# Kernel tuning notes

Hardware: AMD Instinct MI355X
Metric: run time of the kernel (lower is better)

The kernel has to match this reference:

```python
import jax, jax.numpy as jnp
import numpy as np

# irreps multiplicities
MUL0_N, MUL1_N = 64, 32   # node:   64x0e + 32x1o  -> dim 160
MUL0_E, MUL1_E = 8, 8     # edge:    8x0e +  8x1o  -> dim 32
MUL0_H, MUL1_H = 64, 32   # hidden: 64x0e + 32x1o  -> dim 160
N_NODES, N_EDGES = 50000, 800000
D_NODE = MUL0_N + 3 * MUL1_N
D_EDGE = MUL0_E + 3 * MUL1_E
D_HID = MUL0_H + 3 * MUL1_H


def _split(x, mul0, mul1):
    # split flat irreps feature into scalars [.., mul0] and vectors [.., mul1, 3]
    s = x[..., :mul0]
    v = x[..., mul0:].reshape(x.shape[0], mul1, 3)
    return s, v


def fctp_messages(x, e, W1, W2, W3, W4):
    """FullyConnectedTensorProduct(node_irreps, edge_irreps -> hidden_irreps), l<=1.
    Paths: (0e,0e->0e), (1o,1o->0e: delta/sqrt3), (0e,1o->1o), (1o,0e->1o)."""
    xs, xv = _split(x, MUL0_N, MUL1_N)   # [E,64], [E,32,3]
    es, ev = _split(e, MUL0_E, MUL1_E)   # [E,8],  [E,8,3]
    inv_sqrt2 = 1.0 / np.sqrt(2.0)       # 2 paths per output irrep
    s1 = jnp.einsum('ea,eb,abc->ec', xs, es, W1) * (1.0 / np.sqrt(MUL0_N * MUL0_E))
    s2 = jnp.einsum('eai,ebi,abc->ec', xv, ev, W2) * (1.0 / (np.sqrt(3.0) * np.sqrt(MUL1_N * MUL1_E)))
    out_s = (s1 + s2) * inv_sqrt2                         # [E,64]
    v1 = jnp.einsum('ea,ebi,abc->eci', xs, ev, W3) * (1.0 / np.sqrt(MUL0_N * MUL1_E))
    v2 = jnp.einsum('eai,eb,abc->eci', xv, es, W4) * (1.0 / np.sqrt(MUL1_N * MUL0_E))
    out_v = (v1 + v2) * inv_sqrt2                         # [E,32,3]
    return jnp.concatenate([out_s, out_v.reshape(out_v.shape[0], -1)], axis=-1)  # [E,160]


def setup_inputs() -> dict:
    key = jax.random.key(0)
    ks = jax.random.split(key, 12)
    node_features = jax.random.normal(ks[0], (N_NODES, D_NODE), dtype=jnp.float32)
    edge_index = jax.random.randint(ks[1], (2, N_EDGES), 0, N_NODES, dtype=jnp.int64)
    edge_attr_tensor = jax.random.normal(ks[2], (N_EDGES, D_EDGE), dtype=jnp.float32)
    node_attr_scalar_raw = jax.random.normal(ks[3], (N_NODES, 1), dtype=jnp.float32)
    # FCTP path weights (mul_in1, mul_in2, mul_out)
    W1 = jax.random.normal(ks[4], (MUL0_N, MUL0_E, MUL0_H), dtype=jnp.float32)
    W2 = jax.random.normal(ks[5], (MUL1_N, MUL1_E, MUL0_H), dtype=jnp.float32)
    W3 = jax.random.normal(ks[6], (MUL0_N, MUL1_E, MUL1_H), dtype=jnp.float32)
    W4 = jax.random.normal(ks[7], (MUL1_N, MUL0_E, MUL1_H), dtype=jnp.float32)
    # runtime-fallback dense layers (Gate raises at runtime in the original)
    Wm = jax.random.normal(ks[8], (D_HID, D_HID), dtype=jnp.float32) / np.sqrt(D_HID)
    bm = jnp.zeros((D_HID,), dtype=jnp.float32)
    Wu = jax.random.normal(ks[9], (D_NODE + D_HID, D_NODE), dtype=jnp.float32) / np.sqrt(D_NODE + D_HID)
    bu = jnp.zeros((D_NODE,), dtype=jnp.float32)
    return {"node_features": node_features, "edge_index": edge_index,
            "edge_attr_tensor": edge_attr_tensor, "node_attr_scalar_raw": node_attr_scalar_raw,
            "W1": W1, "W2": W2, "W3": W3, "W4": W4,
            "Wm": Wm, "bm": bm, "Wu": Wu, "bu": bu}


def reference(node_features, edge_index, edge_attr_tensor, node_attr_scalar_raw,
              W1, W2, W3, W4, Wm, bm, Wu, bu):
    row, col = edge_index[0], edge_index[1]
    # gather source nodes + equivariant tensor-product message
    tp = fctp_messages(node_features[col], edge_attr_tensor, W1, W2, W3, W4)  # [E,160]
    messages = tp @ Wm + bm                                                   # [E,160]
    # scatter-sum aggregation to destination nodes
    agg = jax.ops.segment_sum(messages, row, num_segments=N_NODES)            # [N,160]
    # update (runtime fallback: linear on concat) + residual
    upd = jnp.concatenate([node_features, agg], axis=-1) @ Wu + bu            # [N,160]
    return node_features + upd
```

## Files before the change

kernel.cpp:

```cpp
#include <hip/hip_runtime.h>
#include <hip/hip_bf16.h>

#define NN 50000
#define NE 800000
#define DN 160
#define DE 32
#define NP 50176

typedef __attribute__((ext_vector_type(2))) _Float16 f16x2;
typedef __attribute__((ext_vector_type(8))) _Float16 f16x8;
typedef __attribute__((ext_vector_type(4))) float f32x4;
typedef __attribute__((ext_vector_type(4))) unsigned short u16x4;

#define R2 0.81649658092772603f
#define R4 1.41421356237309515f
#define SC (1.0f/32.0f)

#define XST 172
#define EST 38

union AF { f16x2 p[4]; f16x8 v; };

__device__ __forceinline__ unsigned short f16bits(float f) {
    union { _Float16 h; unsigned short s; } u;
    u.h = (_Float16)f;
    return u.s;
}

__global__ __launch_bounds__(256) void xprep_kernel(const float* __restrict__ x,
                                                    unsigned short* __restrict__ xb) {
    int i = blockIdx.x * 256 + threadIdx.x;
    if (i < NN * DN / 4) {
        const float4 v = reinterpret_cast<const float4*>(x)[i];
        u16x4 p; p[0] = f16bits(v.x); p[1] = f16bits(v.y); p[2] = f16bits(v.z); p[3] = f16bits(v.w);
        reinterpret_cast<u16x4*>(xb)[i] = p;
    }
}

__global__ __launch_bounds__(256) void zero_kernel(float* __restrict__ T,
                                                   int* __restrict__ cnt) {
    int i = blockIdx.x * 256 + threadIdx.x;
    if (i < NN * DN) T[i] = 0.0f;
    if (i < NP) cnt[i] = 0;
}

__global__ __launch_bounds__(256) void hist_kernel(const int* __restrict__ eidx,
                                                   int* __restrict__ cnt) {
    int e = blockIdx.x * 256 + threadIdx.x;
    if (e < NE) atomicAdd(&cnt[eidx[e]], 1);
}

__global__ __launch_bounds__(256) void scan1_kernel(const int* __restrict__ cnt,
                                                    int* __restrict__ cursor,
                                                    int* __restrict__ bsum) {
    __shared__ int s[256];
    const int t = threadIdx.x;
    const int i = blockIdx.x * 256 + t;
    const int v = cnt[i];
    s[t] = v; __syncthreads();
    for (int off = 1; off < 256; off <<= 1) {
        int u = (t >= off) ? s[t - off] : 0;
        __syncthreads(); s[t] += u; __syncthreads();
    }
    cursor[i] = s[t] - v;
    if (t == 255) bsum[blockIdx.x] = s[255];
}

__global__ __launch_bounds__(256) void scan2_kernel(int* __restrict__ bsum) {
    __shared__ int s[256];
    const int t = threadIdx.x;
    const int v = (t < 196) ? bsum[t] : 0;
    s[t] = v; __syncthreads();
    for (int off = 1; off < 256; off <<= 1) {
        int u = (t >= off) ? s[t - off] : 0;
        __syncthreads(); s[t] += u; __syncthreads();
    }
    if (t < 196) bsum[t] = s[t] - v;
}

__global__ __launch_bounds__(256) void scan3_kernel(int* __restrict__ cursor,
                                                    const int* __restrict__ bsum) {
    int i = blockIdx.x * 256 + threadIdx.x;
    cursor[i] += bsum[blockIdx.x];
}

__global__ __launch_bounds__(256) void scatter_kernel(const int* __restrict__ eidx,
                                                      int* __restrict__ cursor,
                                                      int* __restrict__ sorted) {
    int e = blockIdx.x * 256 + threadIdx.x;
    if (e < NE) {
        int pos = atomicAdd(&cursor[eidx[e]], 1);
        sorted[pos] = e;
    }
}

__global__ __launch_bounds__(256) void wprep_edge_kernel(
    const float* __restrict__ W1, const float* __restrict__ W2,
    const float* __restrict__ W3, const float* __restrict__ W4,
    unsigned short* __restrict__ Wh)
{
    int id = blockIdx.x * 256 + threadIdx.x;
    if (id >= 73728) return;
    int j = id & 7, l = (id >> 3) & 63, st = id >> 9;
    int tt = st / 6, s = st % 6;
    int k = 32 * tt + 8 * (l >> 4) + j;
    float w;
    if (s < 4) {
        int c = s * 16 + (l & 15);
        if (k < 512) { int a = k >> 3, b = k & 7; w = W1[(a*8+b)*64 + c] * SC; }
        else { int k2 = k - 512; int a = k2 >> 3, b = k2 & 7; w = W2[(a*8+b)*64 + c] * (R2*SC); }
    } else {
        int c = (s - 4) * 16 + (l & 15);
        if (k < 512) { int a = k >> 3, b = k & 7; w = W3[(a*8+b)*32 + c] * SC; }
        else { int k2 = k - 512; int a = k2 >> 3, b = k2 & 7; w = W4[(a*8+b)*32 + c] * (R4*SC); }
    }
    Wh[id] = f16bits(w);
}

__global__ __launch_bounds__(256) void wcomp_kernel(
    const float* __restrict__ Wm, const float* __restrict__ bm,
    const float* __restrict__ Wu, float* __restrict__ Wc, float* __restrict__ bc)
{
    int id = blockIdx.x * 256 + threadIdx.x;
    if (id < 160 * 160) {
        int k = id / 160, c = id % 160;
        float s = 0.0f;
        for (int h = 0; h < 160; ++h) s = fmaf(Wm[k*160 + h], Wu[(160 + h)*160 + c], s);
        Wc[id] = s;
    }
    if (id < 160) {
        float s = 0.0f;
        for (int h = 0; h < 160; ++h) s = fmaf(bm[h], Wu[(160 + h)*160 + id], s);
        bc[id] = s;
    }
}

__global__ __launch_bounds__(256) void wprep_node_kernel(
    const float* __restrict__ Wu, const float* __restrict__ Wc,
    unsigned short* __restrict__ Wn)
{
    int id = blockIdx.x * 256 + threadIdx.x;
    if (id >= 51200) return;
    int j = id & 7, l = (id >> 3) & 63, tn = id >> 9;
    int tk = tn % 10, n16 = tn / 10;
    int c = n16 * 16 + (l & 15);
    int k = 32 * tk + 8 * (l >> 4) + j;
    float w;
    if (k < 160) {
        w = Wu[k * 160 + c];
    } else {
        int tcol = k - 160;
        int orig = (tcol < 64) ? tcol : 64 + ((tcol - 64) & 31) * 3 + ((tcol - 64) >> 5);
        w = Wc[orig * 160 + c];
    }
    Wn[id] = f16bits(w);
}

template<int UXB>
__global__ __launch_bounds__(256, 3) void edge_kernel(
    const float* __restrict__ x, const unsigned short* __restrict__ xb,
    const int* __restrict__ eidx, const float* __restrict__ ea,
    const unsigned short* __restrict__ Wh,
    const int* __restrict__ sorted, float* __restrict__ T)
{
    __shared__ __align__(16) char smem[64*XST*2 + 64*EST*2];
    __shared__ int rowls[64];
    __shared__ int colls[64];
    __shared__ int sels[64];

    unsigned short* xls = (unsigned short*)smem;
    unsigned short* els = (unsigned short*)(smem + 64*XST*2);

    const int t = threadIdx.x;
    const int base = blockIdx.x * 64;

    if (t < 64) {
        const int se = sorted[base + t];
        sels[t] = se;
        rowls[t] = eidx[se];
        colls[t] = eidx[NE + se];
    }
    __syncthreads();

    if (UXB) {
        for (int j = t; j < 64 * 40; j += 256) {
            int m = j / 40, q = j - m * 40;
            const u16x4 v = *reinterpret_cast<const u16x4*>(xb + (size_t)colls[m] * DN + q * 4);
            *reinterpret_cast<u16x4*>(&xls[m*XST + q*4]) = v;
        }
    } else {
        for (int j = t; j < 64 * 40; j += 256) {
            int m = j / 40, q = j - m * 40;
            const float4 v = *reinterpret_cast<const float4*>(x + (size_t)colls[m] * DN + q * 4);
            u16x4 p; p[0] = f16bits(v.x); p[1] = f16bits(v.y); p[2] = f16bits(v.z); p[3] = f16bits(v.w);
            *reinterpret_cast<u16x4*>(&xls[m*XST + q*4]) = p;
        }
    }
    for (int j = t; j < 64 * 8; j += 256) {
        int m = j >> 3, q = j & 7;
        const float4 v = *reinterpret_cast<const float4*>(ea + (size_t)sels[m] * DE + q * 4);
        #pragma unroll
        for (int z = 0; z < 4; ++z) {
            int p = q * 4 + z;
            float val = (z == 0) ? v.x : (z == 1) ? v.y : (z == 2) ? v.z : v.w;
            int dst = (p < 8) ? p : 8 + ((p - 8) % 3) * 8 + (p - 8) / 3;
            els[m*EST + dst] = f16bits(val);
        }
    }
    __syncthreads();

    const int lane = t & 63;
    const int wv = t >> 6;
    const int r = lane & 15;
    const int g = lane >> 4;
    const int er = wv * 16 + r;

    f16x2 es2[4], ev2[3][4];
    #pragma unroll
    for (int p = 0; p < 4; ++p) {
        es2[p] = *reinterpret_cast<const f16x2*>(&els[er*EST + 2*p]);
        #pragma unroll
        for (int i = 0; i < 3; ++i)
            ev2[i][p] = *reinterpret_cast<const f16x2*>(&els[er*EST + 8 + i*8 + 2*p]);
    }

    f32x4 accS[4], accV[3][2];
    #pragma unroll
    for (int n = 0; n < 4; ++n) accS[n] = (f32x4){0.f, 0.f, 0.f, 0.f};
    #pragma unroll
    for (int i = 0; i < 3; ++i)
        #pragma unroll
        for (int n = 0; n < 2; ++n) accV[i][n] = (f32x4){0.f, 0.f, 0.f, 0.f};

    const unsigned short* wp = Wh + (size_t)lane * 8;

    for (int tt = 0; tt < 16; ++tt) {
        f16x8 bS0 = *reinterpret_cast<const f16x8*>(wp);
        f16x8 bS1 = *reinterpret_cast<const f16x8*>(wp + 512);
        f16x8 bS2 = *reinterpret_cast<const f16x8*>(wp + 1024);
        f16x8 bS3 = *reinterpret_cast<const f16x8*>(wp + 1536);
        f16x8 bV0 = *reinterpret_cast<const f16x8*>(wp + 2048);
        f16x8 bV1 = *reinterpret_cast<const f16x8*>(wp + 2560);
        wp += 3072;

        const _Float16 xa = *reinterpret_cast<const _Float16*>(&xls[er*XST + 4*tt + g]);
        const f16x2 xa2 = (f16x2){xa, xa};
        AF aS, aV0, aV1, aV2;
        #pragma unroll
        for (int p = 0; p < 4; ++p) {
            aS.p[p]  = xa2 * es2[p];
            aV0.p[p] = xa2 * ev2[0][p];
            aV1.p[p] = xa2 * ev2[1][p];
            aV2.p[p] = xa2 * ev2[2][p];
        }

        accS[0] = __builtin_amdgcn_mfma_f32_16x16x32_f16(aS.v, bS0, accS[0], 0, 0, 0);
        accS[1] = __builtin_amdgcn_mfma_f32_16x16x32_f16(aS.v, bS1, accS[1], 0, 0, 0);
        accS[2] = __builtin_amdgcn_mfma_f32_16x16x32_f16(aS.v, bS2, accS[2], 0, 0, 0);
        accS[3] = __builtin_amdgcn_mfma_f32_16x16x32_f16(aS.v, bS3, accS[3], 0, 0, 0);
        accV[0][0] = __builtin_amdgcn_mfma_f32_16x16x32_f16(aV0.v, bV0, accV[0][0], 0, 0, 0);
        accV[0][1] = __builtin_amdgcn_mfma_f32_16x16x32_f16(aV0.v, bV1, accV[0][1], 0, 0, 0);
        accV[1][0] = __builtin_amdgcn_mfma_f32_16x16x32_f16(aV1.v, bV0, accV[1][0], 0, 0, 0);
        accV[1][1] = __builtin_amdgcn_mfma_f32_16x16x32_f16(aV1.v, bV1, accV[1][1], 0, 0, 0);
        accV[2][0] = __builtin_amdgcn_mfma_f32_16x16x32_f16(aV2.v, bV0, accV[2][0], 0, 0, 0);
        accV[2][1] = __builtin_amdgcn_mfma_f32_16x16x32_f16(aV2.v, bV1, accV[2][1], 0, 0, 0);
    }

    for (int u = 0; u < 8; ++u) {
        f16x8 bS0 = *reinterpret_cast<const f16x8*>(wp);
        f16x8 bS1 = *reinterpret_cast<const f16x8*>(wp + 512);
        f16x8 bS2 = *reinterpret_cast<const f16x8*>(wp + 1024);
        f16x8 bS3 = *reinterpret_cast<const f16x8*>(wp + 1536);
        f16x8 bV0 = *reinterpret_cast<const f16x8*>(wp + 2048);
        f16x8 bV1 = *reinterpret_cast<const f16x8*>(wp + 2560);
        wp += 3072;

        const int a = 4 * u + g;
        const _Float16 x0 = *reinterpret_cast<const _Float16*>(&xls[er*XST + 64 + a*3 + 0]);
        const _Float16 x1 = *reinterpret_cast<const _Float16*>(&xls[er*XST + 64 + a*3 + 1]);
        const _Float16 x2 = *reinterpret_cast<const _Float16*>(&xls[er*XST + 64 + a*3 + 2]);
        const f16x2 x02 = (f16x2){x0, x0};
        const f16x2 x12 = (f16x2){x1, x1};
        const f16x2 x22 = (f16x2){x2, x2};
        AF aS, aV0, aV1, aV2;
        #pragma unroll
        for (int p = 0; p < 4; ++p) {
            f16x2 d = x02 * ev2[0][p];
            d += x12 * ev2[1][p];
            d += x22 * ev2[2][p];
            aS.p[p]  = d;
            aV0.p[p] = x02 * es2[p];
            aV1.p[p] = x12 * es2[p];
            aV2.p[p] = x22 * es2[p];
        }

        accS[0] = __builtin_amdgcn_mfma_f32_16x16x32_f16(aS.v, bS0, accS[0], 0, 0, 0);
        accS[1] = __builtin_amdgcn_mfma_f32_16x16x32_f16(aS.v, bS1, accS[1], 0, 0, 0);
        accS[2] = __builtin_amdgcn_mfma_f32_16x16x32_f16(aS.v, bS2, accS[2], 0, 0, 0);
        accS[3] = __builtin_amdgcn_mfma_f32_16x16x32_f16(aS.v, bS3, accS[3], 0, 0, 0);
        accV[0][0] = __builtin_amdgcn_mfma_f32_16x16x32_f16(aV0.v, bV0, accV[0][0], 0, 0, 0);
        accV[0][1] = __builtin_amdgcn_mfma_f32_16x16x32_f16(aV0.v, bV1, accV[0][1], 0, 0, 0);
        accV[1][0] = __builtin_amdgcn_mfma_f32_16x16x32_f16(aV1.v, bV0, accV[1][0], 0, 0, 0);
        accV[1][1] = __builtin_amdgcn_mfma_f32_16x16x32_f16(aV1.v, bV1, accV[1][1], 0, 0, 0);
        accV[2][0] = __builtin_amdgcn_mfma_f32_16x16x32_f16(aV2.v, bV0, accV[2][0], 0, 0, 0);
        accV[2][1] = __builtin_amdgcn_mfma_f32_16x16x32_f16(aV2.v, bV1, accV[2][1], 0, 0, 0);
    }

    __syncthreads();
    float* accw = (float*)smem;

    #pragma unroll
    for (int half = 0; half < 2; ++half) {
        if ((wv >> 1) == half) {
            const int lbase = (wv & 1) * 16 + g * 4;
            #pragma unroll
            for (int reg = 0; reg < 4; ++reg) {
                const int lrow = lbase + reg;
                #pragma unroll
                for (int n = 0; n < 4; ++n)
                    accw[lrow*161 + n*16 + r] = accS[n][reg];
                #pragma unroll
                for (int i = 0; i < 3; ++i)
                    #pragma unroll
                    for (int n = 0; n < 2; ++n)
                        accw[lrow*161 + 64 + i*32 + n*16 + r] = accV[i][n][reg];
            }
        }
        __syncthreads();

        if (t < DN) {
            const int col = t;
            const int ebase = half * 32;
            float s = 0.0f;
            int rstart = 0;
            for (int e = 0; e < 32; ++e) {
                s += accw[e*161 + col];
                const int ge = ebase + e;
                if (e == 31 || rowls[ge] != rowls[ge + 1]) {
                    float* dst = T + (size_t)rowls[ge] * DN + col;
                    if (rstart == 0 || e == 31) atomicAdd(dst, s);
                    else *dst = s;
                    s = 0.0f; rstart = e + 1;
                }
            }
        }
        __syncthreads();
    }
}

template<int UXB>
__global__ __launch_bounds__(256) void node_kernel(
    const float* __restrict__ x, const unsigned short* __restrict__ xb,
    float* __restrict__ T, const int* __restrict__ cnt,
    const unsigned short* __restrict__ Wn,
    const float* __restrict__ bu, const float* __restrict__ bc)
{
    __shared__ __align__(16) unsigned short A[64][328];
    const int t = threadIdx.x;
    const int nb = blockIdx.x * 64;

    if (UXB) {
        for (int j = t; j < 64 * 40; j += 256) {
            int m = j / 40, q = j - m * 40;
            int row = nb + m; if (row >= NN) row = NN - 1;
            const u16x4 v = *reinterpret_cast<const u16x4*>(xb + (size_t)row * DN + q * 4);
            *reinterpret_cast<u16x4*>(&A[m][q*4]) = v;
        }
    } else {
        for (int j = t; j < 64 * 40; j += 256) {
            int m = j / 40, q = j - m * 40;
            int row = nb + m; if (row >= NN) row = NN - 1;
            const float4 v = *reinterpret_cast<const float4*>(x + (size_t)row * DN + q * 4);
            u16x4 p; p[0] = f16bits(v.x); p[1] = f16bits(v.y); p[2] = f16bits(v.z); p[3] = f16bits(v.w);
            *reinterpret_cast<u16x4*>(&A[m][q*4]) = p;
        }
    }
    for (int j = t; j < 64 * 40; j += 256) {
        int m = j / 40, q = j - m * 40;
        int row = nb + m; if (row >= NN) row = NN - 1;
        const float4 v = *reinterpret_cast<const float4*>(T + (size_t)row * DN + q * 4);
        u16x4 p; p[0] = f16bits(v.x); p[1] = f16bits(v.y); p[2] = f16bits(v.z); p[3] = f16bits(v.w);
        *reinterpret_cast<u16x4*>(&A[m][160 + q*4]) = p;
    }
    __syncthreads();

    const int lane = t & 63;
    const int wv = t >> 6;
    const int r = lane & 15, g = lane >> 4;
    const int er = wv * 16 + r;

    f32x4 acc[10];
    #pragma unroll
    for (int n = 0; n < 10; ++n) acc[n] = (f32x4){0.f, 0.f, 0.f, 0.f};

    for (int tk = 0; tk < 10; ++tk) {
        const f16x8 a = *reinterpret_cast<const f16x8*>(&A[er][32 * tk + 8 * g]);
        #pragma unroll
        for (int n = 0; n < 10; ++n) {
            const f16x8 b = *reinterpret_cast<const f16x8*>(Wn + ((size_t)(n * 10 + tk) * 64 + lane) * 8);
            acc[n] = __builtin_amdgcn_mfma_f32_16x16x32_f16(a, b, acc[n], 0, 0, 0);
        }
    }

    #pragma unroll
    for (int reg = 0; reg < 4; ++reg) {
        const int nrow = nb + wv * 16 + g * 4 + reg;
        if (nrow < NN) {
            const float dg = (float)cnt[nrow];
            #pragma unroll
            for (int n = 0; n < 10; ++n) {
                const int c = n * 16 + r;
                T[(size_t)nrow * DN + c] =
                    acc[n][reg] + x[(size_t)nrow * DN + c] + bu[c] + dg * bc[c];
            }
        }
    }
}

extern "C" void kernel_launch(void* const* d_in, const int* in_sizes, int n_in,
                              void* d_out, int out_size, void* d_ws, size_t ws_size,
                              hipStream_t stream) {
    const float* xf   = (const float*)d_in[0];
    const int*   eidx = (const int*)d_in[1];
    const float* ea   = (const float*)d_in[2];
    const float* W1 = (const float*)d_in[4];
    const float* W2 = (const float*)d_in[5];
    const float* W3 = (const float*)d_in[6];
    const float* W4 = (const float*)d_in[7];
    const float* Wm = (const float*)d_in[8];
    const float* bm = (const float*)d_in[9];
    const float* Wu = (const float*)d_in[10];
    const float* bu = (const float*)d_in[11];

    float* out = (float*)d_out;

    char* ws = (char*)d_ws;
    int*            cnt    = (int*)ws;
    int*            cursor = (int*)(ws + (256 << 10));
    int*            sorted = (int*)(ws + (512 << 10));
    int*            bsum   = (int*)(ws + (3968 << 10));
    unsigned short* Wh     = (unsigned short*)(ws + (4096 << 10));
    float*          Wc     = (float*)(ws + (4352 << 10));
    float*          bc     = (float*)(ws + (4480 << 10));
    unsigned short* Wn     = (unsigned short*)(ws + (4608 << 10));
    unsigned short* xb     = (unsigned short*)(ws + (4864 << 10));

    const bool uxb = ws_size >= ((size_t)(4864 + 16000) << 10);

    wcomp_kernel<<<100, 256, 0, stream>>>(Wm, bm, Wu, Wc, bc);
    wprep_node_kernel<<<200, 256, 0, stream>>>(Wu, Wc, Wn);
    wprep_edge_kernel<<<288, 256, 0, stream>>>(W1, W2, W3, W4, Wh);
    if (uxb) xprep_kernel<<<(NN * DN / 4 + 255) / 256, 256, 0, stream>>>(xf, xb);
    zero_kernel<<<(NN * DN + 255) / 256, 256, 0, stream>>>(out, cnt);
    hist_kernel<<<NE / 256, 256, 0, stream>>>(eidx, cnt);
    scan1_kernel<<<NP / 256, 256, 0, stream>>>(cnt, cursor, bsum);
    scan2_kernel<<<1, 256, 0, stream>>>(bsum);
    scan3_kernel<<<NP / 256, 256, 0, stream>>>(cursor, bsum);
    scatter_kernel<<<NE / 256, 256, 0, stream>>>(eidx, cursor, sorted);
    if (uxb) {
        edge_kernel<1><<<NE / 64, 256, 0, stream>>>(xf, xb, eidx, ea, Wh, sorted, out);
        node_kernel<1><<<(NN + 63) / 64, 256, 0, stream>>>(xf, xb, out, cnt, Wn, bu, bc);
    } else {
        edge_kernel<0><<<NE / 64, 256, 0, stream>>>(xf, xb, eidx, ea, Wh, sorted, out);
        node_kernel<0><<<(NN + 63) / 64, 256, 0, stream>>>(xf, xb, out, cnt, Wn, bu, bc);
    }
}
```

Measured before the change: 514.5 us.

## Switch edge kernel to 32x32x16 MFMA with two waves per block

```diff
diff --git a/kernel.cpp b/kernel.cpp
--- a/kernel.cpp
+++ b/kernel.cpp
@@ -10,6 +10,7 @@
 typedef __attribute__((ext_vector_type(2))) _Float16 f16x2;
 typedef __attribute__((ext_vector_type(8))) _Float16 f16x8;
 typedef __attribute__((ext_vector_type(4))) float f32x4;
+typedef __attribute__((ext_vector_type(16))) float f32x16;
 typedef __attribute__((ext_vector_type(4))) unsigned short u16x4;
 
 #define R2 0.81649658092772603f
@@ -101,18 +102,18 @@
 {
     int id = blockIdx.x * 256 + threadIdx.x;
     if (id >= 73728) return;
-    int j = id & 7, l = (id >> 3) & 63, st = id >> 9;
-    int tt = st / 6, s = st % 6;
-    int k = 32 * tt + 8 * (l >> 4) + j;
+    int j = id & 7, l = (id >> 3) & 63, cs = id >> 9;
+    int c = cs / 3, s = cs % 3;
+    int k = 16 * c + 8 * (l >> 5) + j;
     float w;
-    if (s < 4) {
-        int c = s * 16 + (l & 15);
-        if (k < 512) { int a = k >> 3, b = k & 7; w = W1[(a*8+b)*64 + c] * SC; }
-        else { int k2 = k - 512; int a = k2 >> 3, b = k2 & 7; w = W2[(a*8+b)*64 + c] * (R2*SC); }
+    if (s < 2) {
+        int col = s * 32 + (l & 31);
+        if (k < 512) { int a = k >> 3, b = k & 7; w = W1[(a*8+b)*64 + col] * SC; }
+        else { int k2 = k - 512; int a = k2 >> 3, b = k2 & 7; w = W2[(a*8+b)*64 + col] * (R2*SC); }
     } else {
-        int c = (s - 4) * 16 + (l & 15);
-        if (k < 512) { int a = k >> 3, b = k & 7; w = W3[(a*8+b)*32 + c] * SC; }
-        else { int k2 = k - 512; int a = k2 >> 3, b = k2 & 7; w = W4[(a*8+b)*32 + c] * (R4*SC); }
+        int col = l & 31;
+        if (k < 512) { int a = k >> 3, b = k & 7; w = W3[(a*8+b)*32 + col] * SC; }
+        else { int k2 = k - 512; int a = k2 >> 3, b = k2 & 7; w = W4[(a*8+b)*32 + col] * (R4*SC); }
     }
     Wh[id] = f16bits(w);
 }
@@ -157,7 +158,7 @@
 }
 
 template<int UXB>
-__global__ __launch_bounds__(256, 3) void edge_kernel(
+__global__ __launch_bounds__(128) void edge_kernel(
     const float* __restrict__ x, const unsigned short* __restrict__ xb,
     const int* __restrict__ eidx, const float* __restrict__ ea,
     const unsigned short* __restrict__ Wh,
@@ -183,20 +184,20 @@
     __syncthreads();
 
     if (UXB) {
-        for (int j = t; j < 64 * 40; j += 256) {
+        for (int j = t; j < 64 * 40; j += 128) {
             int m = j / 40, q = j - m * 40;
             const u16x4 v = *reinterpret_cast<const u16x4*>(xb + (size_t)colls[m] * DN + q * 4);
             *reinterpret_cast<u16x4*>(&xls[m*XST + q*4]) = v;
         }
     } else {
-        for (int j = t; j < 64 * 40; j += 256) {
+        for (int j = t; j < 64 * 40; j += 128) {
             int m = j / 40, q = j - m * 40;
             const float4 v = *reinterpret_cast<const float4*>(x + (size_t)colls[m] * DN + q * 4);
             u16x4 p; p[0] = f16bits(v.x); p[1] = f16bits(v.y); p[2] = f16bits(v.z); p[3] = f16bits(v.w);
             *reinterpret_cast<u16x4*>(&xls[m*XST + q*4]) = p;
         }
     }
-    for (int j = t; j < 64 * 8; j += 256) {
+    for (int j = t; j < 64 * 8; j += 128) {
         int m = j >> 3, q = j & 7;
         const float4 v = *reinterpret_cast<const float4*>(ea + (size_t)sels[m] * DE + q * 4);
         #pragma unroll
@@ -211,9 +212,8 @@
 
     const int lane = t & 63;
     const int wv = t >> 6;
-    const int r = lane & 15;
-    const int g = lane >> 4;
-    const int er = wv * 16 + r;
+    const int h = lane >> 5;
+    const int er = wv * 32 + (lane & 31);
 
     f16x2 es2[4], ev2[3][4];
     #pragma unroll
@@ -224,26 +224,17 @@
             ev2[i][p] = *reinterpret_cast<const f16x2*>(&els[er*EST + 8 + i*8 + 2*p]);
     }
 
-    f32x4 accS[4], accV[3][2];
-    #pragma unroll
-    for (int n = 0; n < 4; ++n) accS[n] = (f32x4){0.f, 0.f, 0.f, 0.f};
-    #pragma unroll
-    for (int i = 0; i < 3; ++i)
-        #pragma unroll
-        for (int n = 0; n < 2; ++n) accV[i][n] = (f32x4){0.f, 0.f, 0.f, 0.f};
+    f32x16 accS0 = {}, accS1 = {}, accV[3] = {};
 
     const unsigned short* wp = Wh + (size_t)lane * 8;
 
-    for (int tt = 0; tt < 16; ++tt) {
-        f16x8 bS0 = *reinterpret_cast<const f16x8*>(wp);
-        f16x8 bS1 = *reinterpret_cast<const f16x8*>(wp + 512);
-        f16x8 bS2 = *reinterpret_cast<const f16x8*>(wp + 1024);
-        f16x8 bS3 = *reinterpret_cast<const f16x8*>(wp + 1536);
-        f16x8 bV0 = *reinterpret_cast<const f16x8*>(wp + 2048);
-        f16x8 bV1 = *reinterpret_cast<const f16x8*>(wp + 2560);
-        wp += 3072;
-
-        const _Float16 xa = *reinterpret_cast<const _Float16*>(&xls[er*XST + 4*tt + g]);
+    for (int c = 0; c < 32; ++c) {
+        f16x8 b0 = *reinterpret_cast<const f16x8*>(wp);
+        f16x8 b1 = *reinterpret_cast<const f16x8*>(wp + 512);
+        f16x8 b2 = *reinterpret_cast<const f16x8*>(wp + 1024);
+        wp += 1536;
+
+        const _Float16 xa = *reinterpret_cast<const _Float16*>(&xls[er*XST + 2*c + h]);
         const f16x2 xa2 = (f16x2){xa, xa};
         AF aS, aV0, aV1, aV2;
         #pragma unroll
@@ -254,28 +245,20 @@
             aV2.p[p] = xa2 * ev2[2][p];
         }
 
-        accS[0] = __builtin_amdgcn_mfma_f32_16x16x32_f16(aS.v, bS0, accS[0], 0, 0, 0);
-        accS[1] = __builtin_amdgcn_mfma_f32_16x16x32_f16(aS.v, bS1, accS[1], 0, 0, 0);
-        accS[2] = __builtin_amdgcn_mfma_f32_16x16x32_f16(aS.v, bS2, accS[2], 0, 0, 0);
-        accS[3] = __builtin_amdgcn_mfma_f32_16x16x32_f16(aS.v, bS3, accS[3], 0, 0, 0);
-        accV[0][0] = __builtin_amdgcn_mfma_f32_16x16x32_f16(aV0.v, bV0, accV[0][0], 0, 0, 0);
-        accV[0][1] = __builtin_amdgcn_mfma_f32_16x16x32_f16(aV0.v, bV1, accV[0][1], 0, 0, 0);
-        accV[1][0] = __builtin_amdgcn_mfma_f32_16x16x32_f16(aV1.v, bV0, accV[1][0], 0, 0, 0);
-        accV[1][1] = __builtin_amdgcn_mfma_f32_16x16x32_f16(aV1.v, bV1, accV[1][1], 0, 0, 0);
-        accV[2][0] = __builtin_amdgcn_mfma_f32_16x16x32_f16(aV2.v, bV0, accV[2][0], 0, 0, 0);
-        accV[2][1] = __builtin_amdgcn_mfma_f32_16x16x32_f16(aV2.v, bV1, accV[2][1], 0, 0, 0);
-    }
-
-    for (int u = 0; u < 8; ++u) {
-        f16x8 bS0 = *reinterpret_cast<const f16x8*>(wp);
-        f16x8 bS1 = *reinterpret_cast<const f16x8*>(wp + 512);
-        f16x8 bS2 = *reinterpret_cast<const f16x8*>(wp + 1024);
-        f16x8 bS3 = *reinterpret_cast<const f16x8*>(wp + 1536);
-        f16x8 bV0 = *reinterpret_cast<const f16x8*>(wp + 2048);
-        f16x8 bV1 = *reinterpret_cast<const f16x8*>(wp + 2560);
-        wp += 3072;
-
-        const int a = 4 * u + g;
+        accS0   = __builtin_amdgcn_mfma_f32_32x32x16_f16(aS.v,  b0, accS0,   0, 0, 0);
+        accS1   = __builtin_amdgcn_mfma_f32_32x32x16_f16(aS.v,  b1, accS1,   0, 0, 0);
+        accV[0] = __builtin_amdgcn_mfma_f32_32x32x16_f16(aV0.v, b2, accV[0], 0, 0, 0);
+        accV[1] = __builtin_amdgcn_mfma_f32_32x32x16_f16(aV1.v, b2, accV[1], 0, 0, 0);
+        accV[2] = __builtin_amdgcn_mfma_f32_32x32x16_f16(aV2.v, b2, accV[2], 0, 0, 0);
+    }
+
+    for (int c = 0; c < 16; ++c) {
+        f16x8 b0 = *reinterpret_cast<const f16x8*>(wp);
+        f16x8 b1 = *reinterpret_cast<const f16x8*>(wp + 512);
+        f16x8 b2 = *reinterpret_cast<const f16x8*>(wp + 1024);
+        wp += 1536;
+
+        const int a = 2 * c + h;
         const _Float16 x0 = *reinterpret_cast<const _Float16*>(&xls[er*XST + 64 + a*3 + 0]);
         const _Float16 x1 = *reinterpret_cast<const _Float16*>(&xls[er*XST + 64 + a*3 + 1]);
         const _Float16 x2 = *reinterpret_cast<const _Float16*>(&xls[er*XST + 64 + a*3 + 2]);
@@ -294,16 +277,11 @@
             aV2.p[p] = x22 * es2[p];
         }
 
-        accS[0] = __builtin_amdgcn_mfma_f32_16x16x32_f16(aS.v, bS0, accS[0], 0, 0, 0);
-        accS[1] = __builtin_amdgcn_mfma_f32_16x16x32_f16(aS.v, bS1, accS[1], 0, 0, 0);
-        accS[2] = __builtin_amdgcn_mfma_f32_16x16x32_f16(aS.v, bS2, accS[2], 0, 0, 0);
-        accS[3] = __builtin_amdgcn_mfma_f32_16x16x32_f16(aS.v, bS3, accS[3], 0, 0, 0);
-        accV[0][0] = __builtin_amdgcn_mfma_f32_16x16x32_f16(aV0.v, bV0, accV[0][0], 0, 0, 0);
-        accV[0][1] = __builtin_amdgcn_mfma_f32_16x16x32_f16(aV0.v, bV1, accV[0][1], 0, 0, 0);
-        accV[1][0] = __builtin_amdgcn_mfma_f32_16x16x32_f16(aV1.v, bV0, accV[1][0], 0, 0, 0);
-        accV[1][1] = __builtin_amdgcn_mfma_f32_16x16x32_f16(aV1.v, bV1, accV[1][1], 0, 0, 0);
-        accV[2][0] = __builtin_amdgcn_mfma_f32_16x16x32_f16(aV2.v, bV0, accV[2][0], 0, 0, 0);
-        accV[2][1] = __builtin_amdgcn_mfma_f32_16x16x32_f16(aV2.v, bV1, accV[2][1], 0, 0, 0);
+        accS0   = __builtin_amdgcn_mfma_f32_32x32x16_f16(aS.v,  b0, accS0,   0, 0, 0);
+        accS1   = __builtin_amdgcn_mfma_f32_32x32x16_f16(aS.v,  b1, accS1,   0, 0, 0);
+        accV[0] = __builtin_amdgcn_mfma_f32_32x32x16_f16(aV0.v, b2, accV[0], 0, 0, 0);
+        accV[1] = __builtin_amdgcn_mfma_f32_32x32x16_f16(aV1.v, b2, accV[1], 0, 0, 0);
+        accV[2] = __builtin_amdgcn_mfma_f32_32x32x16_f16(aV2.v, b2, accV[2], 0, 0, 0);
     }
 
     __syncthreads();
@@ -311,36 +289,36 @@
 
     #pragma unroll
     for (int half = 0; half < 2; ++half) {
-        if ((wv >> 1) == half) {
-            const int lbase = (wv & 1) * 16 + g * 4;
+        if (wv == half) {
             #pragma unroll
-            for (int reg = 0; reg < 4; ++reg) {
-                const int lrow = lbase + reg;
-                #pragma unroll
-                for (int n = 0; n < 4; ++n)
-                    accw[lrow*161 + n*16 + r] = accS[n][reg];
+            for (int reg = 0; reg < 16; ++reg) {
+                const int lr = (reg & 3) + 8 * (reg >> 2) + 4 * h;
+                const int cc = lane & 31;
+                accw[lr*161 + cc]      = accS0[reg];
+                accw[lr*161 + 32 + cc] = accS1[reg];
                 #pragma unroll
                 for (int i = 0; i < 3; ++i)
-                    #pragma unroll
-                    for (int n = 0; n < 2; ++n)
-                        accw[lrow*161 + 64 + i*32 + n*16 + r] = accV[i][n][reg];
+                    accw[lr*161 + 64 + i*32 + cc] = accV[i][reg];
             }
         }
         __syncthreads();
 
-        if (t < DN) {
-            const int col = t;
-            const int ebase = half * 32;
-            float s = 0.0f;
-            int rstart = 0;
-            for (int e = 0; e < 32; ++e) {
-                s += accw[e*161 + col];
-                const int ge = ebase + e;
-                if (e == 31 || rowls[ge] != rowls[ge + 1]) {
-                    float* dst = T + (size_t)rowls[ge] * DN + col;
-                    if (rstart == 0 || e == 31) atomicAdd(dst, s);
-                    else *dst = s;
-                    s = 0.0f; rstart = e + 1;
+        #pragma unroll
+        for (int cb = 0; cb < 2; ++cb) {
+            const int col = cb * 128 + t;
+            if (col < DN) {
+                const int ebase = half * 32;
+                float s = 0.0f;
+                int rstart = 0;
+                for (int e = 0; e < 32; ++e) {
+                    s += accw[e*161 + col];
+                    const int ge = ebase + e;
+                    if (e == 31 || rowls[ge] != rowls[ge + 1]) {
+                        float* dst = T + (size_t)rowls[ge] * DN + col;
+                        if (rstart == 0 || e == 31) atomicAdd(dst, s);
+                        else *dst = s;
+                        s = 0.0f; rstart = e + 1;
+                    }
                 }
             }
         }
@@ -458,10 +436,10 @@
     scan3_kernel<<<NP / 256, 256, 0, stream>>>(cursor, bsum);
     scatter_kernel<<<NE / 256, 256, 0, stream>>>(eidx, cursor, sorted);
     if (uxb) {
-        edge_kernel<1><<<NE / 64, 256, 0, stream>>>(xf, xb, eidx, ea, Wh, sorted, out);
+        edge_kernel<1><<<NE / 64, 128, 0, stream>>>(xf, xb, eidx, ea, Wh, sorted, out);
         node_kernel<1><<<(NN + 63) / 64, 256, 0, stream>>>(xf, xb, out, cnt, Wn, bu, bc);
     } else {
-        edge_kernel<0><<<NE / 64, 256, 0, stream>>>(xf, xb, eidx, ea, Wh, sorted, out);
+        edge_kernel<0><<<NE / 64, 128, 0, stream>>>(xf, xb, eidx, ea, Wh, sorted, out);
         node_kernel<0><<<(NN + 63) / 64, 256, 0, stream>>>(xf, xb, out, cnt, Wn, bu, bc);
     }
 }
```

Result: slower. 568.9 us (+10.6%).
